# Optimization experiments

Hardware: AMD Instinct MI355X
Metric: run time of the kernel (lower is better)

The kernel has to match this reference:

```python
import jax, jax.numpy as jnp
import numpy as np

LN_EPS = 1e-5
TOP_K = 2


def _layernorm(x):
    # parameter-free LayerNorm over last dim (elementwise_affine=False)
    mu = jnp.mean(x, axis=-1, keepdims=True)
    var = jnp.var(x, axis=-1, keepdims=True)
    return (x - mu) * jax.lax.rsqrt(var + LN_EPS)


def setup_inputs() -> dict:
    key = jax.random.key(0)
    k1, k2 = jax.random.split(key)
    inp = jax.random.normal(k1, (4, 4096, 2048), dtype=jnp.float32)
    emb = jax.random.normal(k2, (64, 2048), dtype=jnp.float32)
    return {"input": inp, "expert_embeddings": emb}


def reference(input, expert_embeddings):
    # standardize both the tokens and the expert embedding table
    x = _layernorm(input)                      # [b, s, d]
    e = _layernorm(expert_embeddings)          # [E, d]
    sim = jnp.einsum("bsd,ed->bse", x, e)      # [b, s, E]
    temp = jnp.sqrt(jnp.asarray(x.shape[-1], x.dtype))  # t=-1 -> sqrt(d)
    weights, module_indices = jax.lax.top_k(sim, TOP_K)  # [b, s, k]
    gates = jax.nn.softmax(weights / temp, axis=-1)
    return (module_indices, gates)
```

## Files before the change

### kernel.cpp

```cpp
#include <hip/hip_runtime.h>
#include <math.h>

#define D 2048
#define NE 64
#define NTOK 16384
#define KSPLIT 4
#define KRANGE (D / KSPLIT)
#define CHUNK 64
#define NCHUNK (KRANGE / CHUNK)
#define TBLK 64
#define XSTRIDE 65
#define LN_EPS 1e-5f

__global__ __launch_bounds__(256) void expert_ln_kernel(
    const float* __restrict__ emb, float* __restrict__ eT) {
  const int e = blockIdx.x;
  const int tid = threadIdx.x;
  const float4* row = (const float4*)(emb + (size_t)e * D);
  float4 v0 = row[tid * 2];
  float4 v1 = row[tid * 2 + 1];
  float s = v0.x + v0.y + v0.z + v0.w + v1.x + v1.y + v1.z + v1.w;
  float q = v0.x * v0.x + v0.y * v0.y + v0.z * v0.z + v0.w * v0.w
          + v1.x * v1.x + v1.y * v1.y + v1.z * v1.z + v1.w * v1.w;
  #pragma unroll
  for (int off = 32; off > 0; off >>= 1) {
    s += __shfl_down(s, off);
    q += __shfl_down(q, off);
  }
  __shared__ float red[8];
  const int wid = tid >> 6;
  const int lane = tid & 63;
  if (lane == 0) { red[wid] = s; red[4 + wid] = q; }
  __syncthreads();
  if (tid == 0) {
    red[0] = red[0] + red[1] + red[2] + red[3];
    red[4] = red[4] + red[5] + red[6] + red[7];
  }
  __syncthreads();
  const float mu = red[0] * (1.0f / D);
  const float var = red[4] * (1.0f / D) - mu * mu;
  const float sc = rsqrtf(var + LN_EPS);
  float vals[8] = {v0.x, v0.y, v0.z, v0.w, v1.x, v1.y, v1.z, v1.w};
  const int k0 = tid * 8;
  #pragma unroll
  for (int j = 0; j < 8; ++j) {
    eT[(size_t)(k0 + j) * NE + e] = (vals[j] - mu) * sc;
  }
}

__global__ __launch_bounds__(256, 4) void router_gemm_kernel(
    const float* __restrict__ x, const float* __restrict__ eT,
    float* __restrict__ dotP, float* __restrict__ sumP,
    float* __restrict__ sumsqP) {
  __shared__ float xT[CHUNK][XSTRIDE];
  const int tid = threadIdx.x;
  const int bt = blockIdx.x & 255;
  const int kc = blockIdx.x >> 8;
  const int K0 = kc * KRANGE;
  const int lane = tid & 63;
  const int wv = __builtin_amdgcn_readfirstlane(tid >> 6);
  const int ts = tid >> 2;
  const int kb = tid & 3;

  float acc[16];
  #pragma unroll
  for (int j = 0; j < 16; ++j) acc[j] = 0.f;
  float s1 = 0.f, s2 = 0.f;

  const float* xrow = x + (size_t)(bt * TBLK + ts) * D + K0 + kb * 16;

  for (int c = 0; c < NCHUNK; ++c) {
    float4 v[4];
    #pragma unroll
    for (int j = 0; j < 4; ++j) v[j] = *(const float4*)(xrow + c * CHUNK + j * 4);
    __syncthreads();
    #pragma unroll
    for (int j = 0; j < 4; ++j) {
      s1 += v[j].x + v[j].y + v[j].z + v[j].w;
      s2 += v[j].x * v[j].x + v[j].y * v[j].y + v[j].z * v[j].z + v[j].w * v[j].w;
      const int kr = kb * 16 + j * 4;
      xT[kr + 0][ts] = v[j].x;
      xT[kr + 1][ts] = v[j].y;
      xT[kr + 2][ts] = v[j].z;
      xT[kr + 3][ts] = v[j].w;
    }
    __syncthreads();
    const float* ep = eT + (size_t)(K0 + c * CHUNK) * NE + wv * 16;
    #pragma unroll 4
    for (int kk = 0; kk < CHUNK; ++kk) {
      const float xv = xT[kk][lane];
      const float4 e0 = *(const float4*)(ep + (size_t)kk * NE + 0);
      const float4 e1 = *(const float4*)(ep + (size_t)kk * NE + 4);
      const float4 e2 = *(const float4*)(ep + (size_t)kk * NE + 8);
      const float4 e3 = *(const float4*)(ep + (size_t)kk * NE + 12);
      acc[0]  = fmaf(e0.x, xv, acc[0]);
      acc[1]  = fmaf(e0.y, xv, acc[1]);
      acc[2]  = fmaf(e0.z, xv, acc[2]);
      acc[3]  = fmaf(e0.w, xv, acc[3]);
      acc[4]  = fmaf(e1.x, xv, acc[4]);
      acc[5]  = fmaf(e1.y, xv, acc[5]);
      acc[6]  = fmaf(e1.z, xv, acc[6]);
      acc[7]  = fmaf(e1.w, xv, acc[7]);
      acc[8]  = fmaf(e2.x, xv, acc[8]);
      acc[9]  = fmaf(e2.y, xv, acc[9]);
      acc[10] = fmaf(e2.z, xv, acc[10]);
      acc[11] = fmaf(e2.w, xv, acc[11]);
      acc[12] = fmaf(e3.x, xv, acc[12]);
      acc[13] = fmaf(e3.y, xv, acc[13]);
      acc[14] = fmaf(e3.z, xv, acc[14]);
      acc[15] = fmaf(e3.w, xv, acc[15]);
    }
  }

  __syncthreads();
  float* red = &xT[0][0];
  red[kb * 64 + ts] = s1;
  red[256 + kb * 64 + ts] = s2;
  __syncthreads();
  if (tid < TBLK) {
    const int gt = bt * TBLK + tid;
    sumP[kc * NTOK + gt] = red[tid] + red[64 + tid] + red[128 + tid] + red[192 + tid];
    sumsqP[kc * NTOK + gt] =
        red[256 + tid] + red[320 + tid] + red[384 + tid] + red[448 + tid];
  }

  float* dp = dotP + ((size_t)kc * NTOK + (size_t)bt * TBLK + lane) * NE + wv * 16;
  *(float4*)(dp + 0)  = make_float4(acc[0], acc[1], acc[2], acc[3]);
  *(float4*)(dp + 4)  = make_float4(acc[4], acc[5], acc[6], acc[7]);
  *(float4*)(dp + 8)  = make_float4(acc[8], acc[9], acc[10], acc[11]);
  *(float4*)(dp + 12) = make_float4(acc[12], acc[13], acc[14], acc[15]);
}

__global__ __launch_bounds__(256) void finalize_kernel(
    const float* __restrict__ dotP, const float* __restrict__ sumP,
    const float* __restrict__ sumsqP, float* __restrict__ out) {
  const int tid = threadIdx.x;
  const int t = blockIdx.x * 32 + (tid >> 3);
  const int l8 = tid & 7;

  float s1 = 0.f, s2 = 0.f;
  #pragma unroll
  for (int kc = 0; kc < KSPLIT; ++kc) {
    s1 += sumP[kc * NTOK + t];
    s2 += sumsqP[kc * NTOK + t];
  }
  const float mu = s1 * (1.0f / D);
  const float var = s2 * (1.0f / D) - mu * mu;
  const float sc = rsqrtf(var + LN_EPS);

  float d[8] = {0.f, 0.f, 0.f, 0.f, 0.f, 0.f, 0.f, 0.f};
  #pragma unroll
  for (int kc = 0; kc < KSPLIT; ++kc) {
    const float* dp = dotP + ((size_t)kc * NTOK + t) * NE + l8 * 8;
    float4 a = *(const float4*)dp;
    float4 b = *(const float4*)(dp + 4);
    d[0] += a.x; d[1] += a.y; d[2] += a.z; d[3] += a.w;
    d[4] += b.x; d[5] += b.y; d[6] += b.z; d[7] += b.w;
  }

  float w1 = -INFINITY, w2 = -INFINITY;
  int i1 = 0, i2 = 0;
  #pragma unroll
  for (int j = 0; j < 8; ++j) {
    const float v = d[j] * sc;
    const int e = l8 * 8 + j;
    if (v > w1) { w2 = w1; i2 = i1; w1 = v; i1 = e; }
    else if (v > w2) { w2 = v; i2 = e; }
  }
  #pragma unroll
  for (int off = 1; off < 8; off <<= 1) {
    const float ow1 = __shfl_xor(w1, off);
    const float ow2 = __shfl_xor(w2, off);
    const int oi1 = __shfl_xor(i1, off);
    const int oi2 = __shfl_xor(i2, off);
    if (ow1 > w1 || (ow1 == w1 && oi1 < i1)) {
      float nw2; int ni2;
      if (w1 > ow2 || (w1 == ow2 && i1 < oi2)) { nw2 = w1; ni2 = i1; }
      else { nw2 = ow2; ni2 = oi2; }
      w1 = ow1; i1 = oi1; w2 = nw2; i2 = ni2;
    } else {
      if (ow1 > w2 || (ow1 == w2 && oi1 < i2)) { w2 = ow1; i2 = oi1; }
    }
  }

  if (l8 == 0) {
    const float invT = 0.02209708691207961f;
    const float e1 = expf((w2 - w1) * invT);
    const float g1 = 1.0f / (1.0f + e1);
    const float g2 = e1 * g1;
    out[t * 2 + 0] = (float)i1;
    out[t * 2 + 1] = (float)i2;
    out[2 * NTOK + t * 2 + 0] = g1;
    out[2 * NTOK + t * 2 + 1] = g2;
  }
}

extern "C" void kernel_launch(void* const* d_in, const int* in_sizes, int n_in,
                              void* d_out, int out_size, void* d_ws, size_t ws_size,
                              hipStream_t stream) {
  const float* x = (const float*)d_in[0];
  const float* emb = (const float*)d_in[1];
  float* ws = (float*)d_ws;
  float* eT = ws;
  float* dotP = ws + 131072;
  float* sumP = dotP + (size_t)KSPLIT * NTOK * NE;
  float* sumsqP = sumP + (size_t)KSPLIT * NTOK;
  float* out = (float*)d_out;

  expert_ln_kernel<<<NE, 256, 0, stream>>>(emb, eT);
  router_gemm_kernel<<<KSPLIT * (NTOK / TBLK), 256, 0, stream>>>(
      x, eT, dotP, sumP, sumsqP);
  finalize_kernel<<<NTOK / 32, 256, 0, stream>>>(dotP, sumP, sumsqP, out);
}
```

Baseline: 262.6 us.

## Use 4x4 register tiles with shared-memory staged expert chunk and prefetch

Restructures the router GEMM inner loop from one token times 16 experts per thread, with expert rows read from global memory, to a 4x4 register outer product. Both the token tile and the expert chunk are staged in shared memory and read as float4. Global loads for the next chunk are issued before the compute loop to overlap memory latency with FMAs. Chunk size is halved to fit the extra shared buffer, which doubles the number of barrier pairs. The row-sum reduction layout is adjusted to match.

```diff
diff --git a/kernel.cpp b/kernel.cpp
--- a/kernel.cpp
+++ b/kernel.cpp
@@ -6,10 +6,10 @@
 #define NTOK 16384
 #define KSPLIT 4
 #define KRANGE (D / KSPLIT)
-#define CHUNK 64
+#define CHUNK 32
 #define NCHUNK (KRANGE / CHUNK)
 #define TBLK 64
-#define XSTRIDE 65
+#define XPAD 68
 #define LN_EPS 1e-5f
 
 __global__ __launch_bounds__(256) void expert_ln_kernel(
@@ -52,83 +52,101 @@
     const float* __restrict__ x, const float* __restrict__ eT,
     float* __restrict__ dotP, float* __restrict__ sumP,
     float* __restrict__ sumsqP) {
-  __shared__ float xT[CHUNK][XSTRIDE];
+  __shared__ float xT[CHUNK][XPAD];
+  __shared__ float eS[CHUNK][NE];
   const int tid = threadIdx.x;
   const int bt = blockIdx.x & 255;
   const int kc = blockIdx.x >> 8;
   const int K0 = kc * KRANGE;
-  const int lane = tid & 63;
-  const int wv = __builtin_amdgcn_readfirstlane(tid >> 6);
-  const int ts = tid >> 2;
-  const int kb = tid & 3;
-
-  float acc[16];
-  #pragma unroll
-  for (int j = 0; j < 16; ++j) acc[j] = 0.f;
-  float s1 = 0.f, s2 = 0.f;
-
-  const float* xrow = x + (size_t)(bt * TBLK + ts) * D + K0 + kb * 16;
+  const int tg = tid & 15;
+  const int eg = tid >> 4;
+
+  const int stokA = tid >> 3;
+  const int skq = tid & 7;
+  const int sekA = tid >> 4;
+  const int seq = tid & 15;
+
+  float acc[4][4];
+  #pragma unroll
+  for (int i = 0; i < 4; ++i)
+    #pragma unroll
+    for (int j = 0; j < 4; ++j) acc[i][j] = 0.f;
+  float sA = 0.f, qA = 0.f, sB = 0.f, qB = 0.f;
+
+  const float* xbase = x + (size_t)bt * TBLK * D + K0;
+  const float* ebase = eT + (size_t)K0 * NE;
+
+  float4 px0 = *(const float4*)(xbase + (size_t)stokA * D + skq * 4);
+  float4 px1 = *(const float4*)(xbase + (size_t)(stokA + 32) * D + skq * 4);
+  float4 pe0 = *(const float4*)(ebase + (size_t)sekA * NE + seq * 4);
+  float4 pe1 = *(const float4*)(ebase + (size_t)(sekA + 16) * NE + seq * 4);
 
   for (int c = 0; c < NCHUNK; ++c) {
-    float4 v[4];
+    __syncthreads();
+    sA += px0.x + px0.y + px0.z + px0.w;
+    qA += px0.x * px0.x + px0.y * px0.y + px0.z * px0.z + px0.w * px0.w;
+    sB += px1.x + px1.y + px1.z + px1.w;
+    qB += px1.x * px1.x + px1.y * px1.y + px1.z * px1.z + px1.w * px1.w;
+    xT[skq * 4 + 0][stokA] = px0.x;
+    xT[skq * 4 + 1][stokA] = px0.y;
+    xT[skq * 4 + 2][stokA] = px0.z;
+    xT[skq * 4 + 3][stokA] = px0.w;
+    xT[skq * 4 + 0][stokA + 32] = px1.x;
+    xT[skq * 4 + 1][stokA + 32] = px1.y;
+    xT[skq * 4 + 2][stokA + 32] = px1.z;
+    xT[skq * 4 + 3][stokA + 32] = px1.w;
+    *(float4*)&eS[sekA][seq * 4] = pe0;
+    *(float4*)&eS[sekA + 16][seq * 4] = pe1;
+    __syncthreads();
+    if (c + 1 < NCHUNK) {
+      const int off = (c + 1) * CHUNK;
+      px0 = *(const float4*)(xbase + (size_t)stokA * D + off + skq * 4);
+      px1 = *(const float4*)(xbase + (size_t)(stokA + 32) * D + off + skq * 4);
+      pe0 = *(const float4*)(ebase + (size_t)(off + sekA) * NE + seq * 4);
+      pe1 = *(const float4*)(ebase + (size_t)(off + sekA + 16) * NE + seq * 4);
+    }
+    #pragma unroll 8
+    for (int kk = 0; kk < CHUNK; ++kk) {
+      const float4 a = *(const float4*)&xT[kk][tg * 4];
+      const float4 b = *(const float4*)&eS[kk][eg * 4];
+      const float ar[4] = {a.x, a.y, a.z, a.w};
+      const float br[4] = {b.x, b.y, b.z, b.w};
+      #pragma unroll
+      for (int i = 0; i < 4; ++i)
+        #pragma unroll
+        for (int j = 0; j < 4; ++j)
+          acc[i][j] = fmaf(ar[i], br[j], acc[i][j]);
+    }
+  }
+
+  {
+    float* dp = dotP + ((size_t)kc * NTOK + (size_t)bt * TBLK + tg * 4) * NE + eg * 4;
     #pragma unroll
-    for (int j = 0; j < 4; ++j) v[j] = *(const float4*)(xrow + c * CHUNK + j * 4);
-    __syncthreads();
+    for (int i = 0; i < 4; ++i) {
+      *(float4*)(dp + (size_t)i * NE) =
+          make_float4(acc[i][0], acc[i][1], acc[i][2], acc[i][3]);
+    }
+  }
+
+  __syncthreads();
+  float* r1 = &xT[0][0];
+  float* r2 = &xT[0][0] + 512;
+  r1[skq * 64 + stokA] = sA;
+  r1[skq * 64 + 32 + stokA] = sB;
+  r2[skq * 64 + stokA] = qA;
+  r2[skq * 64 + 32 + stokA] = qB;
+  __syncthreads();
+  if (tid < TBLK) {
+    float s = 0.f, q = 0.f;
     #pragma unroll
-    for (int j = 0; j < 4; ++j) {
-      s1 += v[j].x + v[j].y + v[j].z + v[j].w;
-      s2 += v[j].x * v[j].x + v[j].y * v[j].y + v[j].z * v[j].z + v[j].w * v[j].w;
-      const int kr = kb * 16 + j * 4;
-      xT[kr + 0][ts] = v[j].x;
-      xT[kr + 1][ts] = v[j].y;
-      xT[kr + 2][ts] = v[j].z;
-      xT[kr + 3][ts] = v[j].w;
-    }
-    __syncthreads();
-    const float* ep = eT + (size_t)(K0 + c * CHUNK) * NE + wv * 16;
-    #pragma unroll 4
-    for (int kk = 0; kk < CHUNK; ++kk) {
-      const float xv = xT[kk][lane];
-      const float4 e0 = *(const float4*)(ep + (size_t)kk * NE + 0);
-      const float4 e1 = *(const float4*)(ep + (size_t)kk * NE + 4);
-      const float4 e2 = *(const float4*)(ep + (size_t)kk * NE + 8);
-      const float4 e3 = *(const float4*)(ep + (size_t)kk * NE + 12);
-      acc[0]  = fmaf(e0.x, xv, acc[0]);
-      acc[1]  = fmaf(e0.y, xv, acc[1]);
-      acc[2]  = fmaf(e0.z, xv, acc[2]);
-      acc[3]  = fmaf(e0.w, xv, acc[3]);
-      acc[4]  = fmaf(e1.x, xv, acc[4]);
-      acc[5]  = fmaf(e1.y, xv, acc[5]);
-      acc[6]  = fmaf(e1.z, xv, acc[6]);
-      acc[7]  = fmaf(e1.w, xv, acc[7]);
-      acc[8]  = fmaf(e2.x, xv, acc[8]);
-      acc[9]  = fmaf(e2.y, xv, acc[9]);
-      acc[10] = fmaf(e2.z, xv, acc[10]);
-      acc[11] = fmaf(e2.w, xv, acc[11]);
-      acc[12] = fmaf(e3.x, xv, acc[12]);
-      acc[13] = fmaf(e3.y, xv, acc[13]);
-      acc[14] = fmaf(e3.z, xv, acc[14]);
-      acc[15] = fmaf(e3.w, xv, acc[15]);
-    }
-  }
-
-  __syncthreads();
-  float* red = &xT[0][0];
-  red[kb * 64 + ts] = s1;
-  red[256 + kb * 64 + ts] = s2;
-  __syncthreads();
-  if (tid < TBLK) {
+    for (int j = 0; j < 8; ++j) {
+      s += r1[j * 64 + tid];
+      q += r2[j * 64 + tid];
+    }
     const int gt = bt * TBLK + tid;
-    sumP[kc * NTOK + gt] = red[tid] + red[64 + tid] + red[128 + tid] + red[192 + tid];
-    sumsqP[kc * NTOK + gt] =
-        red[256 + tid] + red[320 + tid] + red[384 + tid] + red[448 + tid];
-  }
-
-  float* dp = dotP + ((size_t)kc * NTOK + (size_t)bt * TBLK + lane) * NE + wv * 16;
-  *(float4*)(dp + 0)  = make_float4(acc[0], acc[1], acc[2], acc[3]);
-  *(float4*)(dp + 4)  = make_float4(acc[4], acc[5], acc[6], acc[7]);
-  *(float4*)(dp + 8)  = make_float4(acc[8], acc[9], acc[10], acc[11]);
-  *(float4*)(dp + 12) = make_float4(acc[12], acc[13], acc[14], acc[15]);
+    sumP[kc * NTOK + gt] = s;
+    sumsqP[kc * NTOK + gt] = q;
+  }
 }
 
 __global__ __launch_bounds__(256) void finalize_kernel(
```

Result: faster. 218.5 us (-16.8%).

## Replace FP32 FMA router GEMM with split-bf16 MFMA emulation

Applied to the files above, without the earlier changes.

The token–expert dot products now run on bf16 MFMA instructions. Each fp32 value is split into three bf16 parts (hi/mid/lo), and the six significant cross terms are packed along K so the result keeps near-fp32 accuracy. Expert embeddings are pre-split and pre-tiled in the prep kernel. The main loop double-buffers global loads of the x and B chunks through registers. This removes the scalar FMA bottleneck, at the cost of a 6x larger K on the MFMA side and extra conversion ALU work on x.

```diff
diff --git a/kernel.cpp b/kernel.cpp
--- a/kernel.cpp
+++ b/kernel.cpp
@@ -1,19 +1,33 @@
 #include <hip/hip_runtime.h>
 #include <math.h>
+
+typedef __attribute__((ext_vector_type(8))) short short8;
+typedef __attribute__((ext_vector_type(8))) unsigned short ushort8;
+typedef __attribute__((ext_vector_type(4))) float f32x4;
 
 #define D 2048
 #define NE 64
 #define NTOK 16384
 #define KSPLIT 4
-#define KRANGE (D / KSPLIT)
-#define CHUNK 64
-#define NCHUNK (KRANGE / CHUNK)
-#define TBLK 64
-#define XSTRIDE 65
+#define KRANGE 512
+#define CF32 16
+#define NCHUNK 32
+#define ASTR 104
+#define CHUNK_USH (64 * ASTR)
 #define LN_EPS 1e-5f
 
-__global__ __launch_bounds__(256) void expert_ln_kernel(
-    const float* __restrict__ emb, float* __restrict__ eT) {
+#define BARRIER() asm volatile("s_waitcnt lgkmcnt(0)\n\ts_barrier" ::: "memory")
+
+__device__ __forceinline__ unsigned int bf16rne(float f) {
+  unsigned int u = __builtin_bit_cast(unsigned int, f);
+  return (u + 0x7fffu + ((u >> 16) & 1u)) >> 16;
+}
+__device__ __forceinline__ float bf16tof(unsigned int h) {
+  return __builtin_bit_cast(float, h << 16);
+}
+
+__global__ __launch_bounds__(256) void expert_prep_kernel(
+    const float* __restrict__ emb, unsigned short* __restrict__ B_tiled) {
   const int e = blockIdx.x;
   const int tid = threadIdx.x;
   const float4* row = (const float4*)(emb + (size_t)e * D);
@@ -44,91 +58,133 @@
   const int k0 = tid * 8;
   #pragma unroll
   for (int j = 0; j < 8; ++j) {
-    eT[(size_t)(k0 + j) * NE + e] = (vals[j] - mu) * sc;
-  }
-}
-
-__global__ __launch_bounds__(256, 4) void router_gemm_kernel(
-    const float* __restrict__ x, const float* __restrict__ eT,
+    const int k = k0 + j;
+    const float v = (vals[j] - mu) * sc;
+    const unsigned int eh = bf16rne(v);
+    const float r = v - bf16tof(eh);
+    const unsigned int em = bf16rne(r);
+    const float r2 = r - bf16tof(em);
+    const unsigned int el = bf16rne(r2);
+    unsigned int* du = (unsigned int*)(B_tiled +
+        ((size_t)(k >> 4) * 64 + e) * ASTR + (k & 15) * 6);
+    du[0] = eh | (em << 16);
+    du[1] = eh | (el << 16);
+    du[2] = em | (eh << 16);
+  }
+}
+
+__global__ __launch_bounds__(256, 4) void router_mfma_kernel(
+    const float* __restrict__ x, const unsigned short* __restrict__ B_tiled,
     float* __restrict__ dotP, float* __restrict__ sumP,
     float* __restrict__ sumsqP) {
-  __shared__ float xT[CHUNK][XSTRIDE];
+  __shared__ unsigned short A_s[64 * ASTR];
+  __shared__ unsigned short B_s[64 * ASTR];
   const int tid = threadIdx.x;
   const int bt = blockIdx.x & 255;
   const int kc = blockIdx.x >> 8;
-  const int K0 = kc * KRANGE;
+  const int wid = tid >> 6;
   const int lane = tid & 63;
-  const int wv = __builtin_amdgcn_readfirstlane(tid >> 6);
-  const int ts = tid >> 2;
-  const int kb = tid & 3;
-
-  float acc[16];
-  #pragma unroll
-  for (int j = 0; j < 16; ++j) acc[j] = 0.f;
-  float s1 = 0.f, s2 = 0.f;
-
-  const float* xrow = x + (size_t)(bt * TBLK + ts) * D + K0 + kb * 16;
+  const int wr = wid >> 1;
+  const int wc = wid & 1;
+  const int l15 = lane & 15;
+  const int lh = lane >> 4;
+  const int tok = tid >> 2;
+  const int kq = tid & 3;
+
+  f32x4 acc00 = {0.f, 0.f, 0.f, 0.f};
+  f32x4 acc01 = {0.f, 0.f, 0.f, 0.f};
+  f32x4 acc10 = {0.f, 0.f, 0.f, 0.f};
+  f32x4 acc11 = {0.f, 0.f, 0.f, 0.f};
+  float s1 = 0.f, q1 = 0.f;
+
+  const float* xbase = x + ((size_t)bt * 64 + tok) * D + kc * KRANGE + kq * 4;
+  const unsigned short* btab = B_tiled + (size_t)kc * NCHUNK * CHUNK_USH;
+
+  float4 px = *(const float4*)(xbase);
+  ushort8 pb0 = *(const ushort8*)(btab + tid * 8);
+  ushort8 pb1 = *(const ushort8*)(btab + (tid + 256) * 8);
+  ushort8 pb2 = *(const ushort8*)(btab + (tid + 512) * 8);
+  ushort8 pb3 = {0, 0, 0, 0, 0, 0, 0, 0};
+  if (tid < 64) pb3 = *(const ushort8*)(btab + (tid + 768) * 8);
+
+  const int arow0 = (wr * 32 + l15) * ASTR + lh * 8;
+  const int arow1 = arow0 + 16 * ASTR;
+  const int brow0 = (wc * 32 + l15) * ASTR + lh * 8;
+  const int brow1 = brow0 + 16 * ASTR;
 
   for (int c = 0; c < NCHUNK; ++c) {
-    float4 v[4];
+    BARRIER();
+    {
+      float xv[4] = {px.x, px.y, px.z, px.w};
+      unsigned int* au = (unsigned int*)A_s;
+      const int base_u = tok * 52 + kq * 12;
+      #pragma unroll
+      for (int j = 0; j < 4; ++j) {
+        const float v = xv[j];
+        s1 += v;
+        q1 += v * v;
+        const unsigned int xh = bf16rne(v);
+        const float r = v - bf16tof(xh);
+        const unsigned int xm = bf16rne(r);
+        const float r2 = r - bf16tof(xm);
+        const unsigned int xl = bf16rne(r2);
+        au[base_u + j * 3 + 0] = xh | (xh << 16);
+        au[base_u + j * 3 + 1] = xm | (xh << 16);
+        au[base_u + j * 3 + 2] = xm | (xl << 16);
+      }
+    }
+    *(ushort8*)&B_s[tid * 8] = pb0;
+    *(ushort8*)&B_s[(tid + 256) * 8] = pb1;
+    *(ushort8*)&B_s[(tid + 512) * 8] = pb2;
+    if (tid < 64) *(ushort8*)&B_s[(tid + 768) * 8] = pb3;
+    if (c + 1 < NCHUNK) {
+      px = *(const float4*)(xbase + (c + 1) * CF32);
+      const unsigned short* bsrc = btab + (size_t)(c + 1) * CHUNK_USH;
+      pb0 = *(const ushort8*)(bsrc + tid * 8);
+      pb1 = *(const ushort8*)(bsrc + (tid + 256) * 8);
+      pb2 = *(const ushort8*)(bsrc + (tid + 512) * 8);
+      if (tid < 64) pb3 = *(const ushort8*)(bsrc + (tid + 768) * 8);
+    }
+    BARRIER();
     #pragma unroll
-    for (int j = 0; j < 4; ++j) v[j] = *(const float4*)(xrow + c * CHUNK + j * 4);
-    __syncthreads();
+    for (int ks = 0; ks < 3; ++ks) {
+      const int kk = ks * 32;
+      const short8 a0 = *(const short8*)&A_s[arow0 + kk];
+      const short8 a1 = *(const short8*)&A_s[arow1 + kk];
+      const short8 b0 = *(const short8*)&B_s[brow0 + kk];
+      const short8 b1 = *(const short8*)&B_s[brow1 + kk];
+      acc00 = __builtin_amdgcn_mfma_f32_16x16x32_bf16(a0, b0, acc00, 0, 0, 0);
+      acc01 = __builtin_amdgcn_mfma_f32_16x16x32_bf16(a0, b1, acc01, 0, 0, 0);
+      acc10 = __builtin_amdgcn_mfma_f32_16x16x32_bf16(a1, b0, acc10, 0, 0, 0);
+      acc11 = __builtin_amdgcn_mfma_f32_16x16x32_bf16(a1, b1, acc11, 0, 0, 0);
+    }
+  }
+
+  {
+    float* dp = dotP + ((size_t)kc * NTOK + (size_t)bt * 64) * NE;
+    const int rbase0 = wr * 32 + lh * 4;
+    const int cbase = wc * 32 + l15;
     #pragma unroll
-    for (int j = 0; j < 4; ++j) {
-      s1 += v[j].x + v[j].y + v[j].z + v[j].w;
-      s2 += v[j].x * v[j].x + v[j].y * v[j].y + v[j].z * v[j].z + v[j].w * v[j].w;
-      const int kr = kb * 16 + j * 4;
-      xT[kr + 0][ts] = v[j].x;
-      xT[kr + 1][ts] = v[j].y;
-      xT[kr + 2][ts] = v[j].z;
-      xT[kr + 3][ts] = v[j].w;
-    }
-    __syncthreads();
-    const float* ep = eT + (size_t)(K0 + c * CHUNK) * NE + wv * 16;
-    #pragma unroll 4
-    for (int kk = 0; kk < CHUNK; ++kk) {
-      const float xv = xT[kk][lane];
-      const float4 e0 = *(const float4*)(ep + (size_t)kk * NE + 0);
-      const float4 e1 = *(const float4*)(ep + (size_t)kk * NE + 4);
-      const float4 e2 = *(const float4*)(ep + (size_t)kk * NE + 8);
-      const float4 e3 = *(const float4*)(ep + (size_t)kk * NE + 12);
-      acc[0]  = fmaf(e0.x, xv, acc[0]);
-      acc[1]  = fmaf(e0.y, xv, acc[1]);
-      acc[2]  = fmaf(e0.z, xv, acc[2]);
-      acc[3]  = fmaf(e0.w, xv, acc[3]);
-      acc[4]  = fmaf(e1.x, xv, acc[4]);
-      acc[5]  = fmaf(e1.y, xv, acc[5]);
-      acc[6]  = fmaf(e1.z, xv, acc[6]);
-      acc[7]  = fmaf(e1.w, xv, acc[7]);
-      acc[8]  = fmaf(e2.x, xv, acc[8]);
-      acc[9]  = fmaf(e2.y, xv, acc[9]);
-      acc[10] = fmaf(e2.z, xv, acc[10]);
-      acc[11] = fmaf(e2.w, xv, acc[11]);
-      acc[12] = fmaf(e3.x, xv, acc[12]);
-      acc[13] = fmaf(e3.y, xv, acc[13]);
-      acc[14] = fmaf(e3.z, xv, acc[14]);
-      acc[15] = fmaf(e3.w, xv, acc[15]);
-    }
-  }
-
-  __syncthreads();
-  float* red = &xT[0][0];
-  red[kb * 64 + ts] = s1;
-  red[256 + kb * 64 + ts] = s2;
-  __syncthreads();
-  if (tid < TBLK) {
-    const int gt = bt * TBLK + tid;
-    sumP[kc * NTOK + gt] = red[tid] + red[64 + tid] + red[128 + tid] + red[192 + tid];
-    sumsqP[kc * NTOK + gt] =
-        red[256 + tid] + red[320 + tid] + red[384 + tid] + red[448 + tid];
-  }
-
-  float* dp = dotP + ((size_t)kc * NTOK + (size_t)bt * TBLK + lane) * NE + wv * 16;
-  *(float4*)(dp + 0)  = make_float4(acc[0], acc[1], acc[2], acc[3]);
-  *(float4*)(dp + 4)  = make_float4(acc[4], acc[5], acc[6], acc[7]);
-  *(float4*)(dp + 8)  = make_float4(acc[8], acc[9], acc[10], acc[11]);
-  *(float4*)(dp + 12) = make_float4(acc[12], acc[13], acc[14], acc[15]);
+    for (int r = 0; r < 4; ++r) {
+      dp[(rbase0 + r) * NE + cbase] = acc00[r];
+      dp[(rbase0 + r) * NE + cbase + 16] = acc01[r];
+      dp[(rbase0 + 16 + r) * NE + cbase] = acc10[r];
+      dp[(rbase0 + 16 + r) * NE + cbase + 16] = acc11[r];
+    }
+  }
+
+  BARRIER();
+  float* fl = (float*)A_s;
+  fl[kq * 64 + tok] = s1;
+  fl[256 + kq * 64 + tok] = q1;
+  BARRIER();
+  if (tid < 64) {
+    const float ssum = fl[tid] + fl[64 + tid] + fl[128 + tid] + fl[192 + tid];
+    const float qsum = fl[256 + tid] + fl[320 + tid] + fl[384 + tid] + fl[448 + tid];
+    const int gt = bt * 64 + tid;
+    sumP[kc * NTOK + gt] = ssum;
+    sumsqP[kc * NTOK + gt] = qsum;
+  }
 }
 
 __global__ __launch_bounds__(256) void finalize_kernel(
@@ -200,15 +256,13 @@
                               hipStream_t stream) {
   const float* x = (const float*)d_in[0];
   const float* emb = (const float*)d_in[1];
-  float* ws = (float*)d_ws;
-  float* eT = ws;
-  float* dotP = ws + 131072;
+  unsigned short* B_tiled = (unsigned short*)d_ws;
+  float* dotP = (float*)((char*)d_ws + 2 * 1024 * 1024);
   float* sumP = dotP + (size_t)KSPLIT * NTOK * NE;
   float* sumsqP = sumP + (size_t)KSPLIT * NTOK;
   float* out = (float*)d_out;
 
-  expert_ln_kernel<<<NE, 256, 0, stream>>>(emb, eT);
-  router_gemm_kernel<<<KSPLIT * (NTOK / TBLK), 256, 0, stream>>>(
-      x, eT, dotP, sumP, sumsqP);
+  expert_prep_kernel<<<NE, 256, 0, stream>>>(emb, B_tiled);
+  router_mfma_kernel<<<KSPLIT * 256, 256, 0, stream>>>(x, B_tiled, dotP, sumP, sumsqP);
   finalize_kernel<<<NTOK / 32, 256, 0, stream>>>(dotP, sumP, sumsqP, out);
 }
```

Result: faster. 218.2 us (-16.9%).
